# Performance work log

Hardware: AMD Instinct MI355X
Metric: run time of the kernel (lower is better)

The kernel has to match this reference:

```python
import jax, jax.numpy as jnp
import numpy as np

N, E, ESM, HID, HEADS, L = 50000, 800000, 1280, 256, 8, 3
HD = HID // HEADS  # 32
B, M, AA = 4096, 8, 21
NEG_SLOPE = 0.2
EPS = 1e-5


def setup_inputs() -> dict:
    key = jax.random.key(0)
    ks = jax.random.split(key, 20)
    s = 0.02
    return {
        "x": jax.random.normal(ks[0], (N, ESM), jnp.float32),
        "edge_index": jax.random.randint(ks[1], (2, E), 0, N),
        "sites_padded": jax.random.randint(ks[2], (B, M), 0, N),
        "mut_ids_padded": jax.random.uniform(ks[3], (B, M, AA), jnp.float32),
        "mask": jnp.ones((B, M), dtype=bool),
        "proj_w": jax.random.normal(ks[4], (ESM, HID), jnp.float32) * s,
        "proj_b": jnp.zeros((HID,), jnp.float32),
        "lin_w": jax.random.normal(ks[5], (L, HID, HID), jnp.float32) * s,
        "att_src": jax.random.normal(ks[6], (L, HEADS, HD), jnp.float32) * s,
        "att_dst": jax.random.normal(ks[7], (L, HEADS, HD), jnp.float32) * s,
        "gat_b": jnp.zeros((L, HID), jnp.float32),
        "ln_g": jnp.ones((L, HID), jnp.float32),
        "ln_b": jnp.zeros((L, HID), jnp.float32),
        "pq_w": jax.random.normal(ks[8], (HID + AA, 1), jnp.float32) * s,
        "pq_b": jnp.zeros((1,), jnp.float32),
        "vh_w1": jax.random.normal(ks[9], (HID + AA, HID // 2), jnp.float32) * s,
        "vh_b1": jnp.zeros((HID // 2,), jnp.float32),
        "vh_w2": jax.random.normal(ks[10], (HID // 2, 1), jnp.float32) * s,
        "vh_b2": jnp.zeros((1,), jnp.float32),
    }


def _layer_norm(h, g, b):
    mu = h.mean(-1, keepdims=True)
    var = ((h - mu) ** 2).mean(-1, keepdims=True)
    return (h - mu) * jax.lax.rsqrt(var + EPS) * g + b


def _gat_layer(h, src, dst, lin_w, a_src, a_dst, bias):
    # h: [N, HID]; src/dst: [E+N] (self-loops included)
    xs = (h @ lin_w).reshape(N, HEADS, HD)            # [N, H, D]
    al_s = (xs * a_src).sum(-1)                        # [N, H]
    al_d = (xs * a_dst).sum(-1)                        # [N, H]
    e = al_s[src] + al_d[dst]                          # [E+N, H]
    e = jnp.where(e > 0, e, NEG_SLOPE * e)             # leaky_relu(0.2)
    m = jax.ops.segment_max(e, dst, num_segments=N)    # [N, H]
    ex = jnp.exp(e - m[dst])
    ssum = jax.ops.segment_sum(ex, dst, num_segments=N)
    w = ex / ssum[dst]                                 # softmax over incoming edges
    msg = w[:, :, None] * xs[src]                      # [E+N, H, D]
    out = jax.ops.segment_sum(msg, dst, num_segments=N)
    return out.reshape(N, HID) + bias


def reference(x, edge_index, sites_padded, mut_ids_padded, mask,
              proj_w, proj_b, lin_w, att_src, att_dst, gat_b, ln_g, ln_b,
              pq_w, pq_b, vh_w1, vh_b1, vh_w2, vh_b2):
    # add self-loops (PyG GATConv default)
    loops = jnp.arange(N, dtype=edge_index.dtype)
    src = jnp.concatenate([edge_index[0], loops])
    dst = jnp.concatenate([edge_index[1], loops])

    # encode_graph
    h = x @ proj_w + proj_b
    for i in range(L):
        h_new = _gat_layer(h, src, dst, lin_w[i], att_src[i], att_dst[i], gat_b[i])
        h_new = jax.nn.elu(h_new)
        h = _layer_norm(h_new + h, ln_g[i], ln_b[i])

    # predict_batch
    site_embeds = h[sites_padded]                           # [B, M, HID]
    combined = jnp.concatenate([site_embeds, mut_ids_padded], axis=-1)  # [B, M, HID+21]
    scores = (combined @ pq_w + pq_b)[..., 0]               # [B, M]
    scores = jnp.where(mask, scores, -jnp.inf)
    weights = jax.nn.softmax(scores, axis=-1)[..., None]    # [B, M, 1]
    pooled = (weights * combined).sum(axis=1)               # [B, HID+21]
    hid = jax.nn.relu(pooled @ vh_w1 + vh_b1)               # dropout = identity (eval)
    return (hid @ vh_w2 + vh_b2)[..., 0]                    # [B]
```

## Files before the change

### kernel.cpp

```cpp
#include <hip/hip_runtime.h>
#include <hip/hip_bf16.h>

#define N_NODES 50000
#define N_EDGES 800000
#define ESM_DIM 1280
#define HID_DIM 256
#define N_HEADS 8
#define HD_DIM 32
#define N_LAYERS 3
#define B_SZ 4096
#define M_SZ 8
#define AA_SZ 21

typedef __bf16 bf16x8 __attribute__((ext_vector_type(8)));
typedef float f32x4 __attribute__((ext_vector_type(4)));
typedef unsigned short ushort8 __attribute__((ext_vector_type(8)));
typedef unsigned int uint;
typedef uint uint4v __attribute__((ext_vector_type(4)));

__device__ __forceinline__ float lreluf(float x) { return x > 0.f ? x : 0.2f * x; }
__device__ __forceinline__ float eluf(float x)   { return x > 0.f ? x : expm1f(x); }
__device__ __forceinline__ float b2f(unsigned short u) { return __uint_as_float(((uint)u) << 16); }

__device__ __forceinline__ unsigned short bf16_rne(float f) {
    uint u = __float_as_uint(f);
    uint r = u + 0x7FFFu + ((u >> 16) & 1u);
    return (unsigned short)(r >> 16);
}

__device__ __forceinline__ float waveReduceSum(float v) {
#pragma unroll
    for (int off = 32; off > 0; off >>= 1) v += __shfl_xor(v, off, 64);
    return v;
}

__global__ void wsplit_t(const float* __restrict__ W, unsigned short* __restrict__ BTh,
                         int K, int N) {
    int idx = blockIdx.x * 256 + threadIdx.x;
    if (idx >= K * N) return;
    int k = idx / N, n = idx - k * N;
    BTh[(size_t)n * K + k] = bf16_rne(W[idx]);
}

template<int AF32, int OUTMODE>
__global__ __launch_bounds__(256) void gemm_v6(
    const char* __restrict__ Ap, const unsigned short* __restrict__ BT,
    const float* __restrict__ bias, float* __restrict__ C,
    unsigned short* __restrict__ Cb, int M, int K) {
    constexpr int ABYTES = AF32 ? 16384 : 8192;
    constexpr int STRIDE = ABYTES + 8192;
    constexpr int NA = AF32 ? 4 : 2;
    __shared__ __align__(16) char smem[2 * STRIDE];

    const int tid = threadIdx.x;
    const int bn = blockIdx.x * 128;
    const int bm = blockIdx.y * 128;
    const int wv = tid >> 6, lane = tid & 63;
    const int wr = wv >> 1, wc = wv & 1;
    const int lr = lane & 15, lk = lane >> 4;

    size_t aSrc[NA]; int aDst[NA];
    if constexpr (AF32) {
#pragma unroll
        for (int i = 0; i < 4; ++i) {
            int c = wv + i * 4;
            int rl = c * 8 + (lane >> 3);
            int rg = bm + rl; if (rg >= M) rg = M - 1;
            int g = (lane & 7) ^ (rl & 7);
            aSrc[i] = (size_t)rg * K * 4 + (size_t)g * 16;
            aDst[i] = c * 1024;
        }
    } else {
#pragma unroll
        for (int i = 0; i < 2; ++i) {
            int c = wv + i * 4;
            int rl = c * 16 + (lane >> 2);
            int rg = bm + rl; if (rg >= M) rg = M - 1;
            int g = (lane & 3) ^ ((rl >> 1) & 3);
            aSrc[i] = (size_t)rg * K * 2 + (size_t)g * 16;
            aDst[i] = c * 1024;
        }
    }
    size_t bSrc[2]; int bDst[2];
#pragma unroll
    for (int i = 0; i < 2; ++i) {
        int c = wv + i * 4;
        int rb = c * 16 + (lane >> 2);
        int g = (lane & 3) ^ ((rb >> 1) & 3);
        bSrc[i] = (size_t)(bn + rb) * K * 2 + (size_t)g * 16;
        bDst[i] = c * 1024;
    }

    auto STAGE = [&](int buf, int k0) {
        char* base = smem + buf * STRIDE;
        const size_t ka = (size_t)k0 * (AF32 ? 4 : 2);
        const size_t kb = (size_t)k0 * 2;
#pragma unroll
        for (int i = 0; i < NA; ++i)
            __builtin_amdgcn_global_load_lds(
                (const __attribute__((address_space(1))) void*)(Ap + aSrc[i] + ka),
                (__attribute__((address_space(3))) void*)(base + aDst[i]), 16, 0, 0);
#pragma unroll
        for (int i = 0; i < 2; ++i)
            __builtin_amdgcn_global_load_lds(
                (const __attribute__((address_space(1))) void*)((const char*)BT + bSrc[i] + kb),
                (__attribute__((address_space(3))) void*)(base + ABYTES + bDst[i]), 16, 0, 0);
    };

    f32x4 acc[4][4] = {};
    const int NT = K / 32;
    STAGE(0, 0);
    for (int t = 0; t < NT; ++t) {
        const int cur = t & 1;
        if (t + 1 < NT) {
            STAGE(cur ^ 1, (t + 1) * 32);
            if constexpr (AF32) asm volatile("s_waitcnt vmcnt(6)" ::: "memory");
            else                asm volatile("s_waitcnt vmcnt(4)" ::: "memory");
        } else {
            asm volatile("s_waitcnt vmcnt(0)" ::: "memory");
        }
        __builtin_amdgcn_s_barrier();
        __builtin_amdgcn_sched_barrier(0);

        const char* base = smem + cur * STRIDE;
        bf16x8 ah[4];
        if constexpr (AF32) {
            const float* Af = (const float*)base;
#pragma unroll
            for (int m = 0; m < 4; ++m) {
                int ra = wr * 64 + m * 16 + lr;
                f32x4 f0 = *(const f32x4*)&Af[ra * 32 + (((2 * lk) ^ (ra & 7)) * 4)];
                f32x4 f1 = *(const f32x4*)&Af[ra * 32 + (((2 * lk + 1) ^ (ra & 7)) * 4)];
                uint h0, h1, h2, h3;
                asm("v_cvt_pk_bf16_f32 %0, %1, %2" : "=v"(h0) : "v"(f0[0]), "v"(f0[1]));
                asm("v_cvt_pk_bf16_f32 %0, %1, %2" : "=v"(h1) : "v"(f0[2]), "v"(f0[3]));
                asm("v_cvt_pk_bf16_f32 %0, %1, %2" : "=v"(h2) : "v"(f1[0]), "v"(f1[1]));
                asm("v_cvt_pk_bf16_f32 %0, %1, %2" : "=v"(h3) : "v"(f1[2]), "v"(f1[3]));
                uint4v hv = {h0, h1, h2, h3};
                ah[m] = __builtin_bit_cast(bf16x8, hv);
            }
        } else {
            const unsigned short* Ab = (const unsigned short*)base;
#pragma unroll
            for (int m = 0; m < 4; ++m) {
                int ra = wr * 64 + m * 16 + lr;
                ah[m] = __builtin_bit_cast(bf16x8,
                    *(const ushort8*)&Ab[ra * 32 + ((lk ^ ((ra >> 1) & 3)) * 8)]);
            }
        }
        const unsigned short* Bb = (const unsigned short*)(base + ABYTES);
#pragma unroll
        for (int n = 0; n < 4; ++n) {
            int rb = wc * 64 + n * 16 + lr;
            bf16x8 bh = __builtin_bit_cast(bf16x8,
                *(const ushort8*)&Bb[rb * 32 + ((lk ^ ((rb >> 1) & 3)) * 8)]);
#pragma unroll
            for (int m = 0; m < 4; ++m)
                acc[m][n] = __builtin_amdgcn_mfma_f32_16x16x32_bf16(ah[m], bh, acc[m][n], 0, 0, 0);
        }
        __builtin_amdgcn_sched_barrier(0);
        __builtin_amdgcn_s_barrier();
    }

#pragma unroll
    for (int n = 0; n < 4; ++n) {
        int col = bn + wc * 64 + n * 16 + lr;
        float bi = (OUTMODE == 0 && bias) ? bias[col] : 0.f;
#pragma unroll
        for (int m = 0; m < 4; ++m) {
#pragma unroll
            for (int r = 0; r < 4; ++r) {
                int rowg = bm + wr * 64 + m * 16 + lk * 4 + r;
                if (rowg < M) {
                    float v = acc[m][n][r] + bi;
                    if constexpr (OUTMODE == 0) {
                        C[(size_t)rowg * HID_DIM + col] = v;
                        Cb[(size_t)rowg * HID_DIM + col] = bf16_rne(v);
                    } else {
                        Cb[(size_t)rowg * HID_DIM + col] = bf16_rne(v);
                    }
                }
            }
        }
    }
}

__global__ void att_dots(const unsigned short* __restrict__ xs_b,
                         const float* __restrict__ a_src, const float* __restrict__ a_dst,
                         float* __restrict__ al_s, float* __restrict__ al_d) {
    int idx = blockIdx.x * 256 + threadIdx.x;
    if (idx >= N_NODES * N_HEADS) return;
    int h = idx & 7;
    const ushort8* v = (const ushort8*)(xs_b + (size_t)idx * HD_DIM);
    const float4* as = (const float4*)(a_src + h * HD_DIM);
    const float4* ad = (const float4*)(a_dst + h * HD_DIM);
    float s1 = 0.f, s2 = 0.f;
#pragma unroll
    for (int q = 0; q < 4; ++q) {
        ushort8 xv = v[q];
        float4 a1 = as[2 * q], a1b = as[2 * q + 1];
        float4 a2 = ad[2 * q], a2b = ad[2 * q + 1];
        float x0 = b2f(xv[0]), x1 = b2f(xv[1]), x2 = b2f(xv[2]), x3 = b2f(xv[3]);
        float x4 = b2f(xv[4]), x5 = b2f(xv[5]), x6 = b2f(xv[6]), x7 = b2f(xv[7]);
        s1 += x0 * a1.x + x1 * a1.y + x2 * a1.z + x3 * a1.w
            + x4 * a1b.x + x5 * a1b.y + x6 * a1b.z + x7 * a1b.w;
        s2 += x0 * a2.x + x1 * a2.y + x2 * a2.z + x3 * a2.w
            + x4 * a2b.x + x5 * a2b.y + x6 * a2b.z + x7 * a2b.w;
    }
    al_s[idx] = s1;
    al_d[idx] = s2;
}

__global__ void hist_kernel(const int* __restrict__ dst, int* __restrict__ counts) {
    int e = blockIdx.x * 256 + threadIdx.x;
    if (e < N_EDGES) atomicAdd(&counts[dst[e]], 1);
}

__global__ __launch_bounds__(1024) void scan_kernel(const int* __restrict__ counts,
                                                    int* __restrict__ offsets,
                                                    int* __restrict__ cursor) {
    __shared__ int sums[1024];
    const int t = threadIdx.x;
    const int CH = (N_NODES + 1023) / 1024;
    const int base = t * CH;
    int local = 0;
    for (int i = 0; i < CH; ++i) {
        int idx = base + i;
        if (idx < N_NODES) local += counts[idx];
    }
    sums[t] = local;
    __syncthreads();
    for (int off = 1; off < 1024; off <<= 1) {
        int v = (t >= off) ? sums[t - off] : 0;
        __syncthreads();
        sums[t] += v;
        __syncthreads();
    }
    int run = (t == 0) ? 0 : sums[t - 1];
    for (int i = 0; i < CH; ++i) {
        int idx = base + i;
        if (idx < N_NODES) {
            offsets[idx] = run;
            cursor[idx] = run;
            run += counts[idx];
        }
    }
}

__global__ void scatter_kernel(const int* __restrict__ src, const int* __restrict__ dst,
                               int* __restrict__ cursor, int* __restrict__ csr_src) {
    int e = blockIdx.x * 256 + threadIdx.x;
    if (e < N_EDGES) {
        int d = dst[e];
        int p = atomicAdd(&cursor[d], 1);
        csr_src[p] = src[e];
    }
}

__global__ __launch_bounds__(256) void gat_aggregate(
    const unsigned short* __restrict__ xs_b, const float* __restrict__ al_s,
    const float* __restrict__ al_d,
    const int* __restrict__ offsets, const int* __restrict__ counts,
    const int* __restrict__ csr_src,
    const float* __restrict__ bias, const float* __restrict__ ln_g,
    const float* __restrict__ ln_b,
    const float* __restrict__ h_in, float* __restrict__ h_out,
    unsigned short* __restrict__ hb_out) {
    const int wave = threadIdx.x >> 6;
    const int lane = threadIdx.x & 63;
    const int n = blockIdx.x * 4 + wave;
    if (n >= N_NODES) return;
    const int hh = lane >> 3;
    const float aldn = al_d[n * N_HEADS + hh];
    const float e0 = lreluf(al_s[n * N_HEADS + hh] + aldn);
    const int start = offsets[n];
    const int cnt = counts[n];
    const int* sp = csr_src + start;

    const int es = lane & 7;
    float m = e0;
    for (int j = es; j < cnt; j += 8) {
        int s1 = sp[j];
        m = fmaxf(m, lreluf(al_s[s1 * N_HEADS + hh] + aldn));
    }
    m = fmaxf(m, __shfl_xor(m, 1, 64));
    m = fmaxf(m, __shfl_xor(m, 2, 64));
    m = fmaxf(m, __shfl_xor(m, 4, 64));

    const ushort4* xv4 = (const ushort4*)xs_b;
    float p0 = __expf(e0 - m);
    float s = p0;
    ushort4 x0 = xv4[(size_t)n * 64 + lane];
    float ax = p0 * b2f(x0.x), ay = p0 * b2f(x0.y);
    float az = p0 * b2f(x0.z), aw = p0 * b2f(x0.w);
#pragma unroll 4
    for (int j = 0; j < cnt; ++j) {
        int s1 = sp[j];
        float e = lreluf(al_s[s1 * N_HEADS + hh] + aldn);
        float pj = __expf(e - m);
        ushort4 xr = xv4[(size_t)s1 * 64 + lane];
        s += pj;
        ax += pj * b2f(xr.x);
        ay += pj * b2f(xr.y);
        az += pj * b2f(xr.z);
        aw += pj * b2f(xr.w);
    }
    const float inv = 1.f / s;
    float4 bv = ((const float4*)bias)[lane];
    float4 hp = ((const float4*)h_in)[(size_t)n * 64 + lane];
    float v0 = eluf(ax * inv + bv.x) + hp.x;
    float v1 = eluf(ay * inv + bv.y) + hp.y;
    float v2 = eluf(az * inv + bv.z) + hp.z;
    float v3 = eluf(aw * inv + bv.w) + hp.w;

    float mu = waveReduceSum(v0 + v1 + v2 + v3) * (1.f / 256.f);
    float d0 = v0 - mu, d1 = v1 - mu, d2 = v2 - mu, d3 = v3 - mu;
    float var = waveReduceSum(d0 * d0 + d1 * d1 + d2 * d2 + d3 * d3) * (1.f / 256.f);
    float rstd = rsqrtf(var + 1e-5f);
    float4 g = ((const float4*)ln_g)[lane];
    float4 b2v = ((const float4*)ln_b)[lane];
    float4 outv;
    outv.x = d0 * rstd * g.x + b2v.x;
    outv.y = d1 * rstd * g.y + b2v.y;
    outv.z = d2 * rstd * g.z + b2v.z;
    outv.w = d3 * rstd * g.w + b2v.w;
    ((float4*)h_out)[(size_t)n * 64 + lane] = outv;
    ushort4 ob;
    ob.x = bf16_rne(outv.x); ob.y = bf16_rne(outv.y);
    ob.z = bf16_rne(outv.z); ob.w = bf16_rne(outv.w);
    ((ushort4*)hb_out)[(size_t)n * 64 + lane] = ob;
}

__global__ __launch_bounds__(256) void predict_kernel(
    const float* __restrict__ h, const int* __restrict__ sites,
    const float* __restrict__ muts,
    const float* __restrict__ pq_w, const float* __restrict__ pq_b,
    const float* __restrict__ w1, const float* __restrict__ b1,
    const float* __restrict__ w2, const float* __restrict__ b2,
    float* __restrict__ out) {
    const int wave = threadIdx.x >> 6;
    const int lane = threadIdx.x & 63;
    const int b = blockIdx.x * 4 + wave;
    __shared__ __align__(16) float pooled_s[4][288];

    float scores[M_SZ];
    float4 pv = ((const float4*)pq_w)[lane];
#pragma unroll
    for (int mi = 0; mi < M_SZ; ++mi) {
        int site = sites[b * M_SZ + mi];
        float4 hv = ((const float4*)h)[(size_t)site * 64 + lane];
        float part = hv.x * pv.x + hv.y * pv.y + hv.z * pv.z + hv.w * pv.w;
        if (lane < AA_SZ) part += muts[(size_t)(b * M_SZ + mi) * AA_SZ + lane] * pq_w[256 + lane];
        part = waveReduceSum(part);
        scores[mi] = part + pq_b[0];
    }
    float mx = scores[0];
#pragma unroll
    for (int mi = 1; mi < M_SZ; ++mi) mx = fmaxf(mx, scores[mi]);
    float se = 0.f;
#pragma unroll
    for (int mi = 0; mi < M_SZ; ++mi) { scores[mi] = __expf(scores[mi] - mx); se += scores[mi]; }
    const float inv = 1.f / se;

    float4 pooled = make_float4(0.f, 0.f, 0.f, 0.f);
    float pooledMut = 0.f;
#pragma unroll
    for (int mi = 0; mi < M_SZ; ++mi) {
        int site = sites[b * M_SZ + mi];
        float w = scores[mi] * inv;
        float4 hv = ((const float4*)h)[(size_t)site * 64 + lane];
        pooled.x += w * hv.x; pooled.y += w * hv.y; pooled.z += w * hv.z; pooled.w += w * hv.w;
        if (lane < AA_SZ) pooledMut += w * muts[(size_t)(b * M_SZ + mi) * AA_SZ + lane];
    }
    ((float4*)&pooled_s[wave][0])[lane] = pooled;
    if (lane < AA_SZ) pooled_s[wave][256 + lane] = pooledMut;
    __syncthreads();

    float hid0 = b1[lane], hid1 = b1[lane + 64];
    for (int k = 0; k < HID_DIM + AA_SZ; ++k) {
        float pk = pooled_s[wave][k];
        hid0 += pk * w1[k * 128 + lane];
        hid1 += pk * w1[k * 128 + lane + 64];
    }
    hid0 = fmaxf(hid0, 0.f);
    hid1 = fmaxf(hid1, 0.f);
    float r = hid0 * w2[lane] + hid1 * w2[lane + 64];
    r = waveReduceSum(r);
    if (lane == 0) out[b] = r + b2[0];
}

extern "C" void kernel_launch(void* const* d_in, const int* in_sizes, int n_in,
                              void* d_out, int out_size, void* d_ws, size_t ws_size,
                              hipStream_t stream) {
    const float* x        = (const float*)d_in[0];
    const int*   eidx     = (const int*)d_in[1];
    const int*   sites    = (const int*)d_in[2];
    const float* muts     = (const float*)d_in[3];
    const float* proj_w   = (const float*)d_in[5];
    const float* proj_b   = (const float*)d_in[6];
    const float* lin_w    = (const float*)d_in[7];
    const float* att_src  = (const float*)d_in[8];
    const float* att_dst  = (const float*)d_in[9];
    const float* gat_b    = (const float*)d_in[10];
    const float* ln_g     = (const float*)d_in[11];
    const float* ln_b     = (const float*)d_in[12];
    const float* pq_w     = (const float*)d_in[13];
    const float* pq_b     = (const float*)d_in[14];
    const float* vh_w1    = (const float*)d_in[15];
    const float* vh_b1    = (const float*)d_in[16];
    const float* vh_w2    = (const float*)d_in[17];
    const float* vh_b2    = (const float*)d_in[18];

    char* ws = (char*)d_ws;
    const size_t SZ_H = (size_t)N_NODES * HID_DIM * sizeof(float);
    float* h1   = (float*)ws;                 ws += SZ_H;
    float* h2   = (float*)ws;                 ws += SZ_H;
    unsigned short* hb   = (unsigned short*)ws; ws += (size_t)N_NODES * HID_DIM * 2;
    unsigned short* xs_b = (unsigned short*)ws; ws += (size_t)N_NODES * HID_DIM * 2;
    float* al_s = (float*)ws;                 ws += (size_t)N_NODES * N_HEADS * 4;
    float* al_d = (float*)ws;                 ws += (size_t)N_NODES * N_HEADS * 4;
    int* counts  = (int*)ws;                  ws += 200192;
    int* offsets = (int*)ws;                  ws += 200192;
    int* cursor  = (int*)ws;                  ws += 200192;
    int* csr_src = (int*)ws;                  ws += (size_t)N_EDGES * 4;
    unsigned short* pBTh = (unsigned short*)ws; ws += (size_t)ESM_DIM * HID_DIM * 2;
    unsigned short* lBTh = (unsigned short*)ws; ws += (size_t)N_LAYERS * HID_DIM * HID_DIM * 2;

    const int* e_src = eidx;
    const int* e_dst = eidx + N_EDGES;

    hipMemsetAsync(counts, 0, N_NODES * sizeof(int), stream);
    hist_kernel<<<(N_EDGES + 255) / 256, 256, 0, stream>>>(e_dst, counts);
    scan_kernel<<<1, 1024, 0, stream>>>(counts, offsets, cursor);
    scatter_kernel<<<(N_EDGES + 255) / 256, 256, 0, stream>>>(e_src, e_dst, cursor, csr_src);

    wsplit_t<<<(ESM_DIM * HID_DIM + 255) / 256, 256, 0, stream>>>(proj_w, pBTh, ESM_DIM, HID_DIM);
    for (int l = 0; l < N_LAYERS; ++l) {
        wsplit_t<<<(HID_DIM * HID_DIM + 255) / 256, 256, 0, stream>>>(
            lin_w + (size_t)l * HID_DIM * HID_DIM,
            lBTh + (size_t)l * HID_DIM * HID_DIM, HID_DIM, HID_DIM);
    }

    dim3 gg(HID_DIM / 128, (N_NODES + 127) / 128);
    gemm_v6<1, 0><<<gg, 256, 0, stream>>>((const char*)x, pBTh, proj_b, h1, hb,
                                          N_NODES, ESM_DIM);

    float* hin = h1;
    float* hout = h2;
    for (int l = 0; l < N_LAYERS; ++l) {
        gemm_v6<0, 1><<<gg, 256, 0, stream>>>(
            (const char*)hb, lBTh + (size_t)l * HID_DIM * HID_DIM,
            nullptr, nullptr, xs_b, N_NODES, HID_DIM);
        att_dots<<<(N_NODES * N_HEADS + 255) / 256, 256, 0, stream>>>(
            xs_b, att_src + l * N_HEADS * HD_DIM, att_dst + l * N_HEADS * HD_DIM, al_s, al_d);
        gat_aggregate<<<(N_NODES + 3) / 4, 256, 0, stream>>>(
            xs_b, al_s, al_d, offsets, counts, csr_src,
            gat_b + l * HID_DIM, ln_g + l * HID_DIM, ln_b + l * HID_DIM,
            hin, hout, hb);
        float* t = hin; hin = hout; hout = t;
    }

    predict_kernel<<<B_SZ / 4, 256, 0, stream>>>(
        hin, sites, muts, pq_w, pq_b, vh_w1, vh_b1, vh_w2, vh_b2, (float*)d_out);
}
```

Baseline: 772.0 us.

## Convert fp32 A to bf16 in registers before LDS and remap GEMM tiles per XCD

```diff
diff --git a/kernel.cpp b/kernel.cpp
--- a/kernel.cpp
+++ b/kernel.cpp
@@ -43,33 +43,53 @@
 }
 
 template<int AF32, int OUTMODE>
-__global__ __launch_bounds__(256) void gemm_v6(
+__global__ __launch_bounds__(256) void gemm_v7(
     const char* __restrict__ Ap, const unsigned short* __restrict__ BT,
     const float* __restrict__ bias, float* __restrict__ C,
-    unsigned short* __restrict__ Cb, int M, int K) {
-    constexpr int ABYTES = AF32 ? 16384 : 8192;
-    constexpr int STRIDE = ABYTES + 8192;
-    constexpr int NA = AF32 ? 4 : 2;
-    __shared__ __align__(16) char smem[2 * STRIDE];
+    unsigned short* __restrict__ Cb, int M, int K, int nwg) {
+    __shared__ __align__(16) char smem[4 * 8192];
 
     const int tid = threadIdx.x;
-    const int bn = blockIdx.x * 128;
-    const int bm = blockIdx.y * 128;
+    const int dd = blockIdx.x;
+    const int q = nwg >> 3, r = nwg & 7;
+    const int xcd = dd & 7;
+    const int wg = (xcd < r ? xcd * (q + 1) : r * (q + 1) + (xcd - r) * q) + (dd >> 3);
+    const int bn = (wg & 1) << 7;
+    const int bm = (wg >> 1) << 7;
+
     const int wv = tid >> 6, lane = tid & 63;
     const int wr = wv >> 1, wc = wv & 1;
     const int lr = lane & 15, lk = lane >> 4;
 
-    size_t aSrc[NA]; int aDst[NA];
+    size_t bSrc[2]; int bDst[2];
+#pragma unroll
+    for (int i = 0; i < 2; ++i) {
+        int c = wv + i * 4;
+        int rb = c * 16 + (lane >> 2);
+        int g = (lane & 3) ^ ((rb >> 1) & 3);
+        bSrc[i] = (size_t)(bn + rb) * K * 2 + (size_t)g * 16;
+        bDst[i] = c * 1024;
+    }
+    auto issueB = [&](int buf, int k0) {
+        char* dstbase = smem + 16384 + buf * 8192;
+        const size_t kb = (size_t)k0 * 2;
+#pragma unroll
+        for (int i = 0; i < 2; ++i)
+            __builtin_amdgcn_global_load_lds(
+                (const __attribute__((address_space(1))) void*)((const char*)BT + bSrc[i] + kb),
+                (__attribute__((address_space(3))) void*)(dstbase + bDst[i]), 16, 0, 0);
+    };
+
+    const float* aRowP = nullptr;
+    int aw0 = 0, aw1 = 0;
+    size_t aSrc[2]; int aDst[2];
     if constexpr (AF32) {
-#pragma unroll
-        for (int i = 0; i < 4; ++i) {
-            int c = wv + i * 4;
-            int rl = c * 8 + (lane >> 3);
-            int rg = bm + rl; if (rg >= M) rg = M - 1;
-            int g = (lane & 7) ^ (rl & 7);
-            aSrc[i] = (size_t)rg * K * 4 + (size_t)g * 16;
-            aDst[i] = c * 1024;
-        }
+        const int sr = tid >> 1, sh = tid & 1;
+        int srg = bm + sr; if (srg >= M) srg = M - 1;
+        aRowP = (const float*)Ap + (size_t)srg * K + sh * 16;
+        const uint aswz = (uint)((sr >> 1) & 3);
+        aw0 = sr * 64 + (int)((((uint)(2 * sh)) ^ aswz) * 16);
+        aw1 = sr * 64 + (int)((((uint)(2 * sh + 1)) ^ aswz) * 16);
     } else {
 #pragma unroll
         for (int i = 0; i < 2; ++i) {
@@ -81,85 +101,92 @@
             aDst[i] = c * 1024;
         }
     }
-    size_t bSrc[2]; int bDst[2];
-#pragma unroll
-    for (int i = 0; i < 2; ++i) {
-        int c = wv + i * 4;
-        int rb = c * 16 + (lane >> 2);
-        int g = (lane & 3) ^ ((rb >> 1) & 3);
-        bSrc[i] = (size_t)(bn + rb) * K * 2 + (size_t)g * 16;
-        bDst[i] = c * 1024;
-    }
-
-    auto STAGE = [&](int buf, int k0) {
-        char* base = smem + buf * STRIDE;
-        const size_t ka = (size_t)k0 * (AF32 ? 4 : 2);
-        const size_t kb = (size_t)k0 * 2;
-#pragma unroll
-        for (int i = 0; i < NA; ++i)
+    auto issueA_lds = [&](int buf, int k0) {
+        char* dstbase = smem + buf * 8192;
+        const size_t ka = (size_t)k0 * 2;
+#pragma unroll
+        for (int i = 0; i < 2; ++i)
             __builtin_amdgcn_global_load_lds(
                 (const __attribute__((address_space(1))) void*)(Ap + aSrc[i] + ka),
-                (__attribute__((address_space(3))) void*)(base + aDst[i]), 16, 0, 0);
-#pragma unroll
-        for (int i = 0; i < 2; ++i)
-            __builtin_amdgcn_global_load_lds(
-                (const __attribute__((address_space(1))) void*)((const char*)BT + bSrc[i] + kb),
-                (__attribute__((address_space(3))) void*)(base + ABYTES + bDst[i]), 16, 0, 0);
+                (__attribute__((address_space(3))) void*)(dstbase + aDst[i]), 16, 0, 0);
+    };
+    auto cvtWriteA = [&](int buf, float4 a0, float4 a1, float4 a2, float4 a3) {
+        char* dst = smem + buf * 8192;
+        uint h0, h1, h2, h3, h4, h5, h6, h7;
+        asm("v_cvt_pk_bf16_f32 %0, %1, %2" : "=v"(h0) : "v"(a0.x), "v"(a0.y));
+        asm("v_cvt_pk_bf16_f32 %0, %1, %2" : "=v"(h1) : "v"(a0.z), "v"(a0.w));
+        asm("v_cvt_pk_bf16_f32 %0, %1, %2" : "=v"(h2) : "v"(a1.x), "v"(a1.y));
+        asm("v_cvt_pk_bf16_f32 %0, %1, %2" : "=v"(h3) : "v"(a1.z), "v"(a1.w));
+        asm("v_cvt_pk_bf16_f32 %0, %1, %2" : "=v"(h4) : "v"(a2.x), "v"(a2.y));
+        asm("v_cvt_pk_bf16_f32 %0, %1, %2" : "=v"(h5) : "v"(a2.z), "v"(a2.w));
+        asm("v_cvt_pk_bf16_f32 %0, %1, %2" : "=v"(h6) : "v"(a3.x), "v"(a3.y));
+        asm("v_cvt_pk_bf16_f32 %0, %1, %2" : "=v"(h7) : "v"(a3.z), "v"(a3.w));
+        uint4v v0 = {h0, h1, h2, h3}, v1 = {h4, h5, h6, h7};
+        *(uint4v*)(dst + aw0) = v0;
+        *(uint4v*)(dst + aw1) = v1;
     };
 
     f32x4 acc[4][4] = {};
     const int NT = K / 32;
-    STAGE(0, 0);
+    float4 ar0, ar1, ar2, ar3;
+
+    if constexpr (AF32) {
+        const float4* ap = (const float4*)aRowP;
+        ar0 = ap[0]; ar1 = ap[1]; ar2 = ap[2]; ar3 = ap[3];
+        issueB(0, 0);
+        cvtWriteA(0, ar0, ar1, ar2, ar3);
+        asm volatile("s_waitcnt lgkmcnt(0)" ::: "memory");
+    } else {
+        issueA_lds(0, 0);
+        issueB(0, 0);
+    }
+
     for (int t = 0; t < NT; ++t) {
         const int cur = t & 1;
         if (t + 1 < NT) {
-            STAGE(cur ^ 1, (t + 1) * 32);
-            if constexpr (AF32) asm volatile("s_waitcnt vmcnt(6)" ::: "memory");
-            else                asm volatile("s_waitcnt vmcnt(4)" ::: "memory");
+            const int k0 = (t + 1) * 32;
+            if constexpr (AF32) {
+                const float4* ap = (const float4*)(aRowP + k0);
+                ar0 = ap[0]; ar1 = ap[1]; ar2 = ap[2]; ar3 = ap[3];
+                issueB(cur ^ 1, k0);
+                asm volatile("s_waitcnt vmcnt(6)" ::: "memory");
+            } else {
+                issueA_lds(cur ^ 1, k0);
+                issueB(cur ^ 1, k0);
+                asm volatile("s_waitcnt vmcnt(4)" ::: "memory");
+            }
         } else {
             asm volatile("s_waitcnt vmcnt(0)" ::: "memory");
         }
         __builtin_amdgcn_s_barrier();
         __builtin_amdgcn_sched_barrier(0);
 
-        const char* base = smem + cur * STRIDE;
+        const unsigned short* Abl = (const unsigned short*)(smem + cur * 8192);
+        const unsigned short* Bbl = (const unsigned short*)(smem + 16384 + cur * 8192);
         bf16x8 ah[4];
-        if constexpr (AF32) {
-            const float* Af = (const float*)base;
-#pragma unroll
-            for (int m = 0; m < 4; ++m) {
-                int ra = wr * 64 + m * 16 + lr;
-                f32x4 f0 = *(const f32x4*)&Af[ra * 32 + (((2 * lk) ^ (ra & 7)) * 4)];
-                f32x4 f1 = *(const f32x4*)&Af[ra * 32 + (((2 * lk + 1) ^ (ra & 7)) * 4)];
-                uint h0, h1, h2, h3;
-                asm("v_cvt_pk_bf16_f32 %0, %1, %2" : "=v"(h0) : "v"(f0[0]), "v"(f0[1]));
-                asm("v_cvt_pk_bf16_f32 %0, %1, %2" : "=v"(h1) : "v"(f0[2]), "v"(f0[3]));
-                asm("v_cvt_pk_bf16_f32 %0, %1, %2" : "=v"(h2) : "v"(f1[0]), "v"(f1[1]));
-                asm("v_cvt_pk_bf16_f32 %0, %1, %2" : "=v"(h3) : "v"(f1[2]), "v"(f1[3]));
-                uint4v hv = {h0, h1, h2, h3};
-                ah[m] = __builtin_bit_cast(bf16x8, hv);
-            }
-        } else {
-            const unsigned short* Ab = (const unsigned short*)base;
-#pragma unroll
-            for (int m = 0; m < 4; ++m) {
-                int ra = wr * 64 + m * 16 + lr;
-                ah[m] = __builtin_bit_cast(bf16x8,
-                    *(const ushort8*)&Ab[ra * 32 + ((lk ^ ((ra >> 1) & 3)) * 8)]);
-            }
-        }
-        const unsigned short* Bb = (const unsigned short*)(base + ABYTES);
+#pragma unroll
+        for (int m = 0; m < 4; ++m) {
+            int ra = wr * 64 + m * 16 + lr;
+            ah[m] = __builtin_bit_cast(bf16x8,
+                *(const ushort8*)&Abl[ra * 32 + ((lk ^ ((ra >> 1) & 3)) * 8)]);
+        }
 #pragma unroll
         for (int n = 0; n < 4; ++n) {
             int rb = wc * 64 + n * 16 + lr;
             bf16x8 bh = __builtin_bit_cast(bf16x8,
-                *(const ushort8*)&Bb[rb * 32 + ((lk ^ ((rb >> 1) & 3)) * 8)]);
+                *(const ushort8*)&Bbl[rb * 32 + ((lk ^ ((rb >> 1) & 3)) * 8)]);
 #pragma unroll
             for (int m = 0; m < 4; ++m)
                 acc[m][n] = __builtin_amdgcn_mfma_f32_16x16x32_bf16(ah[m], bh, acc[m][n], 0, 0, 0);
         }
         __builtin_amdgcn_sched_barrier(0);
-        __builtin_amdgcn_s_barrier();
+        if (t + 1 < NT) {
+            if constexpr (AF32) {
+                cvtWriteA(cur ^ 1, ar0, ar1, ar2, ar3);
+                asm volatile("s_waitcnt lgkmcnt(0)" ::: "memory");
+            }
+            __builtin_amdgcn_s_barrier();
+        }
     }
 
 #pragma unroll
@@ -169,10 +196,10 @@
 #pragma unroll
         for (int m = 0; m < 4; ++m) {
 #pragma unroll
-            for (int r = 0; r < 4; ++r) {
-                int rowg = bm + wr * 64 + m * 16 + lk * 4 + r;
+            for (int rr = 0; rr < 4; ++rr) {
+                int rowg = bm + wr * 64 + m * 16 + lk * 4 + rr;
                 if (rowg < M) {
-                    float v = acc[m][n][r] + bi;
+                    float v = acc[m][n][rr] + bi;
                     if constexpr (OUTMODE == 0) {
                         C[(size_t)rowg * HID_DIM + col] = v;
                         Cb[(size_t)rowg * HID_DIM + col] = bf16_rne(v);
@@ -293,7 +320,7 @@
     ushort4 x0 = xv4[(size_t)n * 64 + lane];
     float ax = p0 * b2f(x0.x), ay = p0 * b2f(x0.y);
     float az = p0 * b2f(x0.z), aw = p0 * b2f(x0.w);
-#pragma unroll 4
+#pragma unroll 8
     for (int j = 0; j < cnt; ++j) {
         int s1 = sp[j];
         float e = lreluf(al_s[s1 * N_HEADS + hh] + aldn);
@@ -441,16 +468,16 @@
             lBTh + (size_t)l * HID_DIM * HID_DIM, HID_DIM, HID_DIM);
     }
 
-    dim3 gg(HID_DIM / 128, (N_NODES + 127) / 128);
-    gemm_v6<1, 0><<<gg, 256, 0, stream>>>((const char*)x, pBTh, proj_b, h1, hb,
-                                          N_NODES, ESM_DIM);
+    const int nwg = 2 * ((N_NODES + 127) / 128);
+    gemm_v7<1, 0><<<nwg, 256, 0, stream>>>((const char*)x, pBTh, proj_b, h1, hb,
+                                           N_NODES, ESM_DIM, nwg);
 
     float* hin = h1;
     float* hout = h2;
     for (int l = 0; l < N_LAYERS; ++l) {
-        gemm_v6<0, 1><<<gg, 256, 0, stream>>>(
+        gemm_v7<0, 1><<<nwg, 256, 0, stream>>>(
             (const char*)hb, lBTh + (size_t)l * HID_DIM * HID_DIM,
-            nullptr, nullptr, xs_b, N_NODES, HID_DIM);
+            nullptr, nullptr, xs_b, N_NODES, HID_DIM, nwg);
         att_dots<<<(N_NODES * N_HEADS + 255) / 256, 256, 0, stream>>>(
             xs_b, att_src + l * N_HEADS * HD_DIM, att_dst + l * N_HEADS * HD_DIM, al_s, al_d);
         gat_aggregate<<<(N_NODES + 3) / 4, 256, 0, stream>>>(
```

New measurement: 805.4 us. 4.3% more time.

## Store projected features head-major and split aggregation into per-head pass plus LN epilogue

Applied to the files above, without the earlier changes.

```diff
diff --git a/kernel.cpp b/kernel.cpp
--- a/kernel.cpp
+++ b/kernel.cpp
@@ -43,18 +43,23 @@
 }
 
 template<int AF32, int OUTMODE>
-__global__ __launch_bounds__(256) void gemm_v6(
+__global__ __launch_bounds__(256) void gemm_v8(
     const char* __restrict__ Ap, const unsigned short* __restrict__ BT,
     const float* __restrict__ bias, float* __restrict__ C,
-    unsigned short* __restrict__ Cb, int M, int K) {
+    unsigned short* __restrict__ Cb, int M, int K, int nwg) {
     constexpr int ABYTES = AF32 ? 16384 : 8192;
     constexpr int STRIDE = ABYTES + 8192;
     constexpr int NA = AF32 ? 4 : 2;
     __shared__ __align__(16) char smem[2 * STRIDE];
 
     const int tid = threadIdx.x;
-    const int bn = blockIdx.x * 128;
-    const int bm = blockIdx.y * 128;
+    const int dd = blockIdx.x;
+    const int q = nwg >> 3, r = nwg & 7;
+    const int xcd = dd & 7;
+    const int wg = (xcd < r ? xcd * (q + 1) : r * (q + 1) + (xcd - r) * q) + (dd >> 3);
+    const int bn = (wg & 1) << 7;
+    const int bm = (wg >> 1) << 7;
+
     const int wv = tid >> 6, lane = tid & 63;
     const int wr = wv >> 1, wc = wv & 1;
     const int lr = lane & 15, lk = lane >> 4;
@@ -169,15 +174,15 @@
 #pragma unroll
         for (int m = 0; m < 4; ++m) {
 #pragma unroll
-            for (int r = 0; r < 4; ++r) {
-                int rowg = bm + wr * 64 + m * 16 + lk * 4 + r;
+            for (int rr = 0; rr < 4; ++rr) {
+                int rowg = bm + wr * 64 + m * 16 + lk * 4 + rr;
                 if (rowg < M) {
-                    float v = acc[m][n][r] + bi;
+                    float v = acc[m][n][rr] + bi;
                     if constexpr (OUTMODE == 0) {
                         C[(size_t)rowg * HID_DIM + col] = v;
                         Cb[(size_t)rowg * HID_DIM + col] = bf16_rne(v);
                     } else {
-                        Cb[(size_t)rowg * HID_DIM + col] = bf16_rne(v);
+                        Cb[((size_t)(col >> 5) * N_NODES + rowg) * 32 + (col & 31)] = bf16_rne(v);
                     }
                 }
             }
@@ -185,13 +190,13 @@
     }
 }
 
-__global__ void att_dots(const unsigned short* __restrict__ xs_b,
+__global__ void att_dots(const unsigned short* __restrict__ xs_hm,
                          const float* __restrict__ a_src, const float* __restrict__ a_dst,
-                         float* __restrict__ al_s, float* __restrict__ al_d) {
+                         float* __restrict__ als_hm, float* __restrict__ ald_hm) {
     int idx = blockIdx.x * 256 + threadIdx.x;
     if (idx >= N_NODES * N_HEADS) return;
-    int h = idx & 7;
-    const ushort8* v = (const ushort8*)(xs_b + (size_t)idx * HD_DIM);
+    int h = idx / N_NODES;
+    const ushort8* v = (const ushort8*)(xs_hm + (size_t)idx * HD_DIM);
     const float4* as = (const float4*)(a_src + h * HD_DIM);
     const float4* ad = (const float4*)(a_dst + h * HD_DIM);
     float s1 = 0.f, s2 = 0.f;
@@ -207,8 +212,8 @@
         s2 += x0 * a2.x + x1 * a2.y + x2 * a2.z + x3 * a2.w
             + x4 * a2b.x + x5 * a2b.y + x6 * a2b.z + x7 * a2b.w;
     }
-    al_s[idx] = s1;
-    al_d[idx] = s2;
+    als_hm[idx] = s1;
+    ald_hm[idx] = s2;
 }
 
 __global__ void hist_kernel(const int* __restrict__ dst, int* __restrict__ counts) {
@@ -257,61 +262,66 @@
     }
 }
 
-__global__ __launch_bounds__(256) void gat_aggregate(
-    const unsigned short* __restrict__ xs_b, const float* __restrict__ al_s,
-    const float* __restrict__ al_d,
+__global__ __launch_bounds__(256) void gat_headpass(
+    const unsigned short* __restrict__ xs_hm, const float* __restrict__ als_hm,
+    const float* __restrict__ ald_hm,
     const int* __restrict__ offsets, const int* __restrict__ counts,
-    const int* __restrict__ csr_src,
-    const float* __restrict__ bias, const float* __restrict__ ln_g,
-    const float* __restrict__ ln_b,
-    const float* __restrict__ h_in, float* __restrict__ h_out,
-    unsigned short* __restrict__ hb_out) {
+    const int* __restrict__ csr_src, unsigned short* __restrict__ msg) {
+    const int wave = threadIdx.x >> 6;
+    const int lane = threadIdx.x & 63;
+    const int n = blockIdx.x * 4 + wave;
+    const int hy = blockIdx.y;
+    if (n >= N_NODES) return;
+    const int par = lane >> 5, d = lane & 31;
+    const float* als = als_hm + (size_t)hy * N_NODES;
+    const unsigned short* xsl = xs_hm + (size_t)hy * N_NODES * 32;
+    const float aldn = ald_hm[(size_t)hy * N_NODES + n];
+    const float e0 = lreluf(als[n] + aldn);
+    const int start = offsets[n];
+    const int cnt = counts[n];
+    const int* sp = csr_src + start;
+
+    float m = e0;
+    for (int j = lane; j < cnt; j += 64)
+        m = fmaxf(m, lreluf(als[sp[j]] + aldn));
+#pragma unroll
+    for (int off = 32; off > 0; off >>= 1) m = fmaxf(m, __shfl_xor(m, off, 64));
+
+    float p0 = __expf(e0 - m);
+    float acc = (par == 0) ? p0 * b2f(xsl[(size_t)n * 32 + d]) : 0.f;
+    float s   = (par == 0) ? p0 : 0.f;
+#pragma unroll 4
+    for (int j0 = 0; j0 < cnt; j0 += 2) {
+        int j = j0 + par;
+        bool valid = j < cnt;
+        int src = sp[valid ? j : cnt - 1];
+        float e = lreluf(als[src] + aldn);
+        float pj = valid ? __expf(e - m) : 0.f;
+        float xv = b2f(xsl[(size_t)src * 32 + d]);
+        acc += pj * xv;
+        s += pj;
+    }
+    acc += __shfl_xor(acc, 32, 64);
+    s   += __shfl_xor(s, 32, 64);
+    float rmsg = acc / s;
+    if (par == 0) msg[(size_t)n * HID_DIM + hy * 32 + d] = bf16_rne(rmsg);
+}
+
+__global__ __launch_bounds__(256) void ln_epilogue(
+    const unsigned short* __restrict__ msg, const float* __restrict__ bias,
+    const float* __restrict__ ln_g, const float* __restrict__ ln_b,
+    float* __restrict__ h, unsigned short* __restrict__ hb_out) {
     const int wave = threadIdx.x >> 6;
     const int lane = threadIdx.x & 63;
     const int n = blockIdx.x * 4 + wave;
     if (n >= N_NODES) return;
-    const int hh = lane >> 3;
-    const float aldn = al_d[n * N_HEADS + hh];
-    const float e0 = lreluf(al_s[n * N_HEADS + hh] + aldn);
-    const int start = offsets[n];
-    const int cnt = counts[n];
-    const int* sp = csr_src + start;
-
-    const int es = lane & 7;
-    float m = e0;
-    for (int j = es; j < cnt; j += 8) {
-        int s1 = sp[j];
-        m = fmaxf(m, lreluf(al_s[s1 * N_HEADS + hh] + aldn));
-    }
-    m = fmaxf(m, __shfl_xor(m, 1, 64));
-    m = fmaxf(m, __shfl_xor(m, 2, 64));
-    m = fmaxf(m, __shfl_xor(m, 4, 64));
-
-    const ushort4* xv4 = (const ushort4*)xs_b;
-    float p0 = __expf(e0 - m);
-    float s = p0;
-    ushort4 x0 = xv4[(size_t)n * 64 + lane];
-    float ax = p0 * b2f(x0.x), ay = p0 * b2f(x0.y);
-    float az = p0 * b2f(x0.z), aw = p0 * b2f(x0.w);
-#pragma unroll 4
-    for (int j = 0; j < cnt; ++j) {
-        int s1 = sp[j];
-        float e = lreluf(al_s[s1 * N_HEADS + hh] + aldn);
-        float pj = __expf(e - m);
-        ushort4 xr = xv4[(size_t)s1 * 64 + lane];
-        s += pj;
-        ax += pj * b2f(xr.x);
-        ay += pj * b2f(xr.y);
-        az += pj * b2f(xr.z);
-        aw += pj * b2f(xr.w);
-    }
-    const float inv = 1.f / s;
+    ushort4 mv = ((const ushort4*)msg)[(size_t)n * 64 + lane];
     float4 bv = ((const float4*)bias)[lane];
-    float4 hp = ((const float4*)h_in)[(size_t)n * 64 + lane];
-    float v0 = eluf(ax * inv + bv.x) + hp.x;
-    float v1 = eluf(ay * inv + bv.y) + hp.y;
-    float v2 = eluf(az * inv + bv.z) + hp.z;
-    float v3 = eluf(aw * inv + bv.w) + hp.w;
+    float4 hp = ((const float4*)h)[(size_t)n * 64 + lane];
+    float v0 = eluf(b2f(mv.x) + bv.x) + hp.x;
+    float v1 = eluf(b2f(mv.y) + bv.y) + hp.y;
+    float v2 = eluf(b2f(mv.z) + bv.z) + hp.z;
+    float v3 = eluf(b2f(mv.w) + bv.w) + hp.w;
 
     float mu = waveReduceSum(v0 + v1 + v2 + v3) * (1.f / 256.f);
     float d0 = v0 - mu, d1 = v1 - mu, d2 = v2 - mu, d3 = v3 - mu;
@@ -324,7 +334,7 @@
     outv.y = d1 * rstd * g.y + b2v.y;
     outv.z = d2 * rstd * g.z + b2v.z;
     outv.w = d3 * rstd * g.w + b2v.w;
-    ((float4*)h_out)[(size_t)n * 64 + lane] = outv;
+    ((float4*)h)[(size_t)n * 64 + lane] = outv;
     ushort4 ob;
     ob.x = bf16_rne(outv.x); ob.y = bf16_rne(outv.y);
     ob.z = bf16_rne(outv.z); ob.w = bf16_rne(outv.w);
@@ -412,17 +422,16 @@
     const float* vh_b2    = (const float*)d_in[18];
 
     char* ws = (char*)d_ws;
-    const size_t SZ_H = (size_t)N_NODES * HID_DIM * sizeof(float);
-    float* h1   = (float*)ws;                 ws += SZ_H;
-    float* h2   = (float*)ws;                 ws += SZ_H;
-    unsigned short* hb   = (unsigned short*)ws; ws += (size_t)N_NODES * HID_DIM * 2;
-    unsigned short* xs_b = (unsigned short*)ws; ws += (size_t)N_NODES * HID_DIM * 2;
-    float* al_s = (float*)ws;                 ws += (size_t)N_NODES * N_HEADS * 4;
-    float* al_d = (float*)ws;                 ws += (size_t)N_NODES * N_HEADS * 4;
-    int* counts  = (int*)ws;                  ws += 200192;
-    int* offsets = (int*)ws;                  ws += 200192;
-    int* cursor  = (int*)ws;                  ws += 200192;
-    int* csr_src = (int*)ws;                  ws += (size_t)N_EDGES * 4;
+    float* h1   = (float*)ws;                   ws += (size_t)N_NODES * HID_DIM * 4;
+    unsigned short* hb    = (unsigned short*)ws; ws += (size_t)N_NODES * HID_DIM * 2;
+    unsigned short* xs_hm = (unsigned short*)ws; ws += (size_t)N_NODES * HID_DIM * 2;
+    unsigned short* msg   = (unsigned short*)ws; ws += (size_t)N_NODES * HID_DIM * 2;
+    float* als_hm = (float*)ws;                 ws += (size_t)N_NODES * N_HEADS * 4;
+    float* ald_hm = (float*)ws;                 ws += (size_t)N_NODES * N_HEADS * 4;
+    int* counts  = (int*)ws;                    ws += 200192;
+    int* offsets = (int*)ws;                    ws += 200192;
+    int* cursor  = (int*)ws;                    ws += 200192;
+    int* csr_src = (int*)ws;                    ws += (size_t)N_EDGES * 4;
     unsigned short* pBTh = (unsigned short*)ws; ws += (size_t)ESM_DIM * HID_DIM * 2;
     unsigned short* lBTh = (unsigned short*)ws; ws += (size_t)N_LAYERS * HID_DIM * HID_DIM * 2;
 
@@ -441,25 +450,25 @@
             lBTh + (size_t)l * HID_DIM * HID_DIM, HID_DIM, HID_DIM);
     }
 
-    dim3 gg(HID_DIM / 128, (N_NODES + 127) / 128);
-    gemm_v6<1, 0><<<gg, 256, 0, stream>>>((const char*)x, pBTh, proj_b, h1, hb,
-                                          N_NODES, ESM_DIM);
-
-    float* hin = h1;
-    float* hout = h2;
+    const int nwg = 2 * ((N_NODES + 127) / 128);
+    gemm_v8<1, 0><<<nwg, 256, 0, stream>>>((const char*)x, pBTh, proj_b, h1, hb,
+                                           N_NODES, ESM_DIM, nwg);
+
+    dim3 hg((N_NODES + 3) / 4, N_HEADS);
     for (int l = 0; l < N_LAYERS; ++l) {
-        gemm_v6<0, 1><<<gg, 256, 0, stream>>>(
+        gemm_v8<0, 1><<<nwg, 256, 0, stream>>>(
             (const char*)hb, lBTh + (size_t)l * HID_DIM * HID_DIM,
-            nullptr, nullptr, xs_b, N_NODES, HID_DIM);
+            nullptr, nullptr, xs_hm, N_NODES, HID_DIM, nwg);
         att_dots<<<(N_NODES * N_HEADS + 255) / 256, 256, 0, stream>>>(
-            xs_b, att_src + l * N_HEADS * HD_DIM, att_dst + l * N_HEADS * HD_DIM, al_s, al_d);
-        gat_aggregate<<<(N_NODES + 3) / 4, 256, 0, stream>>>(
-            xs_b, al_s, al_d, offsets, counts, csr_src,
-            gat_b + l * HID_DIM, ln_g + l * HID_DIM, ln_b + l * HID_DIM,
-            hin, hout, hb);
-        float* t = hin; hin = hout; hout = t;
+            xs_hm, att_src + l * N_HEADS * HD_DIM, att_dst + l * N_HEADS * HD_DIM,
+            als_hm, ald_hm);
+        gat_headpass<<<hg, 256, 0, stream>>>(
+            xs_hm, als_hm, ald_hm, offsets, counts, csr_src, msg);
+        ln_epilogue<<<(N_NODES + 3) / 4, 256, 0, stream>>>(
+            msg, gat_b + l * HID_DIM, ln_g + l * HID_DIM, ln_b + l * HID_DIM,
+            h1, hb);
     }
 
     predict_kernel<<<B_SZ / 4, 256, 0, stream>>>(
-        hin, sites, muts, pq_w, pq_b, vh_w1, vh_b1, vh_w2, vh_b2, (float*)d_out);
-}
+        h1, sites, muts, pq_w, pq_b, vh_w1, vh_b1, vh_w2, vh_b2, (float*)d_out);
+}
```

After: 1.235 ms. 60.0% more time.

## Split GAT softmax into node-max and edge-weight kernels, remap GEMM blocks per XCD

Applied to the files above, without the earlier changes.

```diff
diff --git a/kernel.cpp b/kernel.cpp
--- a/kernel.cpp
+++ b/kernel.cpp
@@ -43,18 +43,23 @@
 }
 
 template<int AF32, int OUTMODE>
-__global__ __launch_bounds__(256) void gemm_v6(
+__global__ __launch_bounds__(256) void gemm_v8(
     const char* __restrict__ Ap, const unsigned short* __restrict__ BT,
     const float* __restrict__ bias, float* __restrict__ C,
-    unsigned short* __restrict__ Cb, int M, int K) {
+    unsigned short* __restrict__ Cb, int M, int K, int nwg) {
     constexpr int ABYTES = AF32 ? 16384 : 8192;
     constexpr int STRIDE = ABYTES + 8192;
     constexpr int NA = AF32 ? 4 : 2;
     __shared__ __align__(16) char smem[2 * STRIDE];
 
     const int tid = threadIdx.x;
-    const int bn = blockIdx.x * 128;
-    const int bm = blockIdx.y * 128;
+    const int dd = blockIdx.x;
+    const int q = nwg >> 3, r = nwg & 7;
+    const int xcd = dd & 7;
+    const int wg = (xcd < r ? xcd * (q + 1) : r * (q + 1) + (xcd - r) * q) + (dd >> 3);
+    const int bn = (wg & 1) << 7;
+    const int bm = (wg >> 1) << 7;
+
     const int wv = tid >> 6, lane = tid & 63;
     const int wr = wv >> 1, wc = wv & 1;
     const int lr = lane & 15, lk = lane >> 4;
@@ -169,10 +174,10 @@
 #pragma unroll
         for (int m = 0; m < 4; ++m) {
 #pragma unroll
-            for (int r = 0; r < 4; ++r) {
-                int rowg = bm + wr * 64 + m * 16 + lk * 4 + r;
+            for (int rr = 0; rr < 4; ++rr) {
+                int rowg = bm + wr * 64 + m * 16 + lk * 4 + rr;
                 if (rowg < M) {
-                    float v = acc[m][n][r] + bi;
+                    float v = acc[m][n][rr] + bi;
                     if constexpr (OUTMODE == 0) {
                         C[(size_t)rowg * HID_DIM + col] = v;
                         Cb[(size_t)rowg * HID_DIM + col] = bf16_rne(v);
@@ -248,66 +253,92 @@
 }
 
 __global__ void scatter_kernel(const int* __restrict__ src, const int* __restrict__ dst,
-                               int* __restrict__ cursor, int* __restrict__ csr_src) {
+                               int* __restrict__ cursor, int* __restrict__ csr_src,
+                               int* __restrict__ csr_dst) {
     int e = blockIdx.x * 256 + threadIdx.x;
     if (e < N_EDGES) {
         int d = dst[e];
         int p = atomicAdd(&cursor[d], 1);
         csr_src[p] = src[e];
-    }
+        csr_dst[p] = d;
+    }
+}
+
+__global__ __launch_bounds__(256) void node_max(
+    const float* __restrict__ al_s, const float* __restrict__ al_d,
+    const int* __restrict__ offsets, const int* __restrict__ counts,
+    const int* __restrict__ csr_src, float* __restrict__ mbuf) {
+    const int wave = threadIdx.x >> 6;
+    const int lane = threadIdx.x & 63;
+    const int n = blockIdx.x * 4 + wave;
+    if (n >= N_NODES) return;
+    const int hh = lane >> 3, es = lane & 7;
+    const float aldn = al_d[n * N_HEADS + hh];
+    float m = lreluf(al_s[n * N_HEADS + hh] + aldn);
+    const int start = offsets[n];
+    const int cnt = counts[n];
+    const int* sp = csr_src + start;
+    for (int j = es; j < cnt; j += 8)
+        m = fmaxf(m, lreluf(al_s[sp[j] * N_HEADS + hh] + aldn));
+    m = fmaxf(m, __shfl_xor(m, 1, 64));
+    m = fmaxf(m, __shfl_xor(m, 2, 64));
+    m = fmaxf(m, __shfl_xor(m, 4, 64));
+    if (es == 0) mbuf[n * N_HEADS + hh] = m;
+}
+
+__global__ void edge_weights(
+    const float* __restrict__ al_s, const float* __restrict__ al_d,
+    const float* __restrict__ mbuf, const int* __restrict__ csr_src,
+    const int* __restrict__ csr_dst, float* __restrict__ wbuf) {
+    int idx = blockIdx.x * 256 + threadIdx.x;
+    if (idx >= N_EDGES * N_HEADS) return;
+    int slot = idx >> 3, h = idx & 7;
+    int src = csr_src[slot], dst = csr_dst[slot];
+    float e = lreluf(al_s[src * N_HEADS + h] + al_d[dst * N_HEADS + h]);
+    wbuf[idx] = __expf(e - mbuf[dst * N_HEADS + h]);
 }
 
 __global__ __launch_bounds__(256) void gat_aggregate(
     const unsigned short* __restrict__ xs_b, const float* __restrict__ al_s,
-    const float* __restrict__ al_d,
+    const float* __restrict__ al_d, const float* __restrict__ mbuf,
+    const float* __restrict__ wbuf,
     const int* __restrict__ offsets, const int* __restrict__ counts,
     const int* __restrict__ csr_src,
     const float* __restrict__ bias, const float* __restrict__ ln_g,
     const float* __restrict__ ln_b,
-    const float* __restrict__ h_in, float* __restrict__ h_out,
-    unsigned short* __restrict__ hb_out) {
+    float* __restrict__ h, unsigned short* __restrict__ hb_out) {
     const int wave = threadIdx.x >> 6;
     const int lane = threadIdx.x & 63;
     const int n = blockIdx.x * 4 + wave;
     if (n >= N_NODES) return;
     const int hh = lane >> 3;
-    const float aldn = al_d[n * N_HEADS + hh];
-    const float e0 = lreluf(al_s[n * N_HEADS + hh] + aldn);
     const int start = offsets[n];
     const int cnt = counts[n];
     const int* sp = csr_src + start;
-
-    const int es = lane & 7;
-    float m = e0;
-    for (int j = es; j < cnt; j += 8) {
-        int s1 = sp[j];
-        m = fmaxf(m, lreluf(al_s[s1 * N_HEADS + hh] + aldn));
-    }
-    m = fmaxf(m, __shfl_xor(m, 1, 64));
-    m = fmaxf(m, __shfl_xor(m, 2, 64));
-    m = fmaxf(m, __shfl_xor(m, 4, 64));
+    const float* wp = wbuf + (size_t)start * N_HEADS;
+
+    const float e0 = lreluf(al_s[n * N_HEADS + hh] + al_d[n * N_HEADS + hh]);
+    float w0 = __expf(e0 - mbuf[n * N_HEADS + hh]);
 
     const ushort4* xv4 = (const ushort4*)xs_b;
-    float p0 = __expf(e0 - m);
-    float s = p0;
+    float s = w0;
     ushort4 x0 = xv4[(size_t)n * 64 + lane];
-    float ax = p0 * b2f(x0.x), ay = p0 * b2f(x0.y);
-    float az = p0 * b2f(x0.z), aw = p0 * b2f(x0.w);
+    float ax = w0 * b2f(x0.x), ay = w0 * b2f(x0.y);
+    float az = w0 * b2f(x0.z), aw = w0 * b2f(x0.w);
 #pragma unroll 4
     for (int j = 0; j < cnt; ++j) {
         int s1 = sp[j];
-        float e = lreluf(al_s[s1 * N_HEADS + hh] + aldn);
-        float pj = __expf(e - m);
+        float wv = wp[j * N_HEADS + hh];
         ushort4 xr = xv4[(size_t)s1 * 64 + lane];
-        s += pj;
-        ax += pj * b2f(xr.x);
-        ay += pj * b2f(xr.y);
-        az += pj * b2f(xr.z);
-        aw += pj * b2f(xr.w);
+        s += wv;
+        ax += wv * b2f(xr.x);
+        ay += wv * b2f(xr.y);
+        az += wv * b2f(xr.z);
+        aw += wv * b2f(xr.w);
     }
     const float inv = 1.f / s;
     float4 bv = ((const float4*)bias)[lane];
-    float4 hp = ((const float4*)h_in)[(size_t)n * 64 + lane];
+    float4 hp = ((const float4*)h)[(size_t)n * 64 + lane];
     float v0 = eluf(ax * inv + bv.x) + hp.x;
     float v1 = eluf(ay * inv + bv.y) + hp.y;
     float v2 = eluf(az * inv + bv.z) + hp.z;
@@ -324,7 +355,7 @@
     outv.y = d1 * rstd * g.y + b2v.y;
     outv.z = d2 * rstd * g.z + b2v.z;
     outv.w = d3 * rstd * g.w + b2v.w;
-    ((float4*)h_out)[(size_t)n * 64 + lane] = outv;
+    ((float4*)h)[(size_t)n * 64 + lane] = outv;
     ushort4 ob;
     ob.x = bf16_rne(outv.x); ob.y = bf16_rne(outv.y);
     ob.z = bf16_rne(outv.z); ob.w = bf16_rne(outv.w);
@@ -412,17 +443,18 @@
     const float* vh_b2    = (const float*)d_in[18];
 
     char* ws = (char*)d_ws;
-    const size_t SZ_H = (size_t)N_NODES * HID_DIM * sizeof(float);
-    float* h1   = (float*)ws;                 ws += SZ_H;
-    float* h2   = (float*)ws;                 ws += SZ_H;
+    float* h1   = (float*)ws;                   ws += (size_t)N_NODES * HID_DIM * 4;
     unsigned short* hb   = (unsigned short*)ws; ws += (size_t)N_NODES * HID_DIM * 2;
     unsigned short* xs_b = (unsigned short*)ws; ws += (size_t)N_NODES * HID_DIM * 2;
-    float* al_s = (float*)ws;                 ws += (size_t)N_NODES * N_HEADS * 4;
-    float* al_d = (float*)ws;                 ws += (size_t)N_NODES * N_HEADS * 4;
-    int* counts  = (int*)ws;                  ws += 200192;
-    int* offsets = (int*)ws;                  ws += 200192;
-    int* cursor  = (int*)ws;                  ws += 200192;
-    int* csr_src = (int*)ws;                  ws += (size_t)N_EDGES * 4;
+    float* al_s = (float*)ws;                   ws += (size_t)N_NODES * N_HEADS * 4;
+    float* al_d = (float*)ws;                   ws += (size_t)N_NODES * N_HEADS * 4;
+    float* mbuf = (float*)ws;                   ws += (size_t)N_NODES * N_HEADS * 4;
+    float* wbuf = (float*)ws;                   ws += (size_t)N_EDGES * N_HEADS * 4;
+    int* counts  = (int*)ws;                    ws += 200192;
+    int* offsets = (int*)ws;                    ws += 200192;
+    int* cursor  = (int*)ws;                    ws += 200192;
+    int* csr_src = (int*)ws;                    ws += (size_t)N_EDGES * 4;
+    int* csr_dst = (int*)ws;                    ws += (size_t)N_EDGES * 4;
     unsigned short* pBTh = (unsigned short*)ws; ws += (size_t)ESM_DIM * HID_DIM * 2;
     unsigned short* lBTh = (unsigned short*)ws; ws += (size_t)N_LAYERS * HID_DIM * HID_DIM * 2;
 
@@ -432,7 +464,8 @@
     hipMemsetAsync(counts, 0, N_NODES * sizeof(int), stream);
     hist_kernel<<<(N_EDGES + 255) / 256, 256, 0, stream>>>(e_dst, counts);
     scan_kernel<<<1, 1024, 0, stream>>>(counts, offsets, cursor);
-    scatter_kernel<<<(N_EDGES + 255) / 256, 256, 0, stream>>>(e_src, e_dst, cursor, csr_src);
+    scatter_kernel<<<(N_EDGES + 255) / 256, 256, 0, stream>>>(e_src, e_dst, cursor,
+                                                              csr_src, csr_dst);
 
     wsplit_t<<<(ESM_DIM * HID_DIM + 255) / 256, 256, 0, stream>>>(proj_w, pBTh, ESM_DIM, HID_DIM);
     for (int l = 0; l < N_LAYERS; ++l) {
@@ -441,25 +474,27 @@
             lBTh + (size_t)l * HID_DIM * HID_DIM, HID_DIM, HID_DIM);
     }
 
-    dim3 gg(HID_DIM / 128, (N_NODES + 127) / 128);
-    gemm_v6<1, 0><<<gg, 256, 0, stream>>>((const char*)x, pBTh, proj_b, h1, hb,
-                                          N_NODES, ESM_DIM);
-
-    float* hin = h1;
-    float* hout = h2;
+    const int nwg = 2 * ((N_NODES + 127) / 128);
+    gemm_v8<1, 0><<<nwg, 256, 0, stream>>>((const char*)x, pBTh, proj_b, h1, hb,
+                                           N_NODES, ESM_DIM, nwg);
+
+    const int ng4 = (N_NODES + 3) / 4;
     for (int l = 0; l < N_LAYERS; ++l) {
-        gemm_v6<0, 1><<<gg, 256, 0, stream>>>(
+        gemm_v8<0, 1><<<nwg, 256, 0, stream>>>(
             (const char*)hb, lBTh + (size_t)l * HID_DIM * HID_DIM,
-            nullptr, nullptr, xs_b, N_NODES, HID_DIM);
+            nullptr, nullptr, xs_b, N_NODES, HID_DIM, nwg);
         att_dots<<<(N_NODES * N_HEADS + 255) / 256, 256, 0, stream>>>(
-            xs_b, att_src + l * N_HEADS * HD_DIM, att_dst + l * N_HEADS * HD_DIM, al_s, al_d);
-        gat_aggregate<<<(N_NODES + 3) / 4, 256, 0, stream>>>(
-            xs_b, al_s, al_d, offsets, counts, csr_src,
+            xs_b, att_src + l * N_HEADS * HD_DIM, att_dst + l * N_HEADS * HD_DIM,
+            al_s, al_d);
+        node_max<<<ng4, 256, 0, stream>>>(al_s, al_d, offsets, counts, csr_src, mbuf);
+        edge_weights<<<(N_EDGES * N_HEADS + 255) / 256, 256, 0, stream>>>(
+            al_s, al_d, mbuf, csr_src, csr_dst, wbuf);
+        gat_aggregate<<<ng4, 256, 0, stream>>>(
+            xs_b, al_s, al_d, mbuf, wbuf, offsets, counts, csr_src,
             gat_b + l * HID_DIM, ln_g + l * HID_DIM, ln_b + l * HID_DIM,
-            hin, hout, hb);
-        float* t = hin; hin = hout; hout = t;
+            h1, hb);
     }
 
     predict_kernel<<<B_SZ / 4, 256, 0, stream>>>(
-        hin, sites, muts, pq_w, pq_b, vh_w1, vh_b1, vh_w2, vh_b2, (float*)d_out);
-}
+        h1, sites, muts, pq_w, pq_b, vh_w1, vh_b1, vh_w2, vh_b2, (float*)d_out);
+}
```

After: 834.0 us. 8.0% more time.
